# Optimization experiments

Measured on AMD Instinct MI355X. Metric: run time of the kernel, lower is better.

## Reference

```python
import jax, jax.numpy as jnp
import numpy as np

N = 102400       # total nodes (1024 graphs x 100 nodes)
E = 1638400      # edges (avg degree 16)
B = 1024         # graphs; also GRU sequence length (unbatched 2D GRU input)
F_IN, HID, H1 = 4, 16, 6
OUT, FC1, RNN, ACT = 32, 64, 64, 11


def _gat(x, src, dst, W, a_src, a_dst, b, heads, out_dim, concat):
    # PyG GATConv (eval mode, dropout off), add_self_loops=True
    n = x.shape[0]
    loop = jnp.arange(n, dtype=src.dtype)
    s = jnp.concatenate([src, loop])
    d = jnp.concatenate([dst, loop])
    h = (x @ W.T).reshape(n, heads, out_dim)                 # [N,H,F]
    a_s = (h * a_src).sum(-1)                                # [N,H]
    a_d = (h * a_dst).sum(-1)                                # [N,H]
    e = jax.nn.leaky_relu(a_s[s] + a_d[d], 0.2)              # [E',H]
    m = jax.ops.segment_max(e, d, num_segments=n)
    p = jnp.exp(e - m[d])
    alpha = p / jax.ops.segment_sum(p, d, num_segments=n)[d]
    agg = jax.ops.segment_sum(h[s] * alpha[:, :, None], d, num_segments=n)  # [N,H,F]
    agg = agg.reshape(n, heads * out_dim) if concat else agg.mean(axis=1)
    return agg + b


def _gru(xs, wih, whh, bih, bhh):
    # torch nn.GRU, unbatched: xs is [L, FC1], h0 = zeros
    def step(hp, xt):
        gi = xt @ wih.T + bih
        gh = hp @ whh.T + bhh
        ir, iz, i_n = jnp.split(gi, 3)
        hr, hz, h_n = jnp.split(gh, 3)
        r = jax.nn.sigmoid(ir + hr)
        z = jax.nn.sigmoid(iz + hz)
        ng = jnp.tanh(i_n + r * h_n)
        h = (1.0 - z) * ng + z * hp
        return h, h
    _, ys = jax.lax.scan(step, jnp.zeros((RNN,), xs.dtype), xs)
    return ys


def setup_inputs():
    key = jax.random.key(0)
    ks = jax.random.split(key, 16)
    g = lambda i, shape, fan: jax.random.normal(ks[i], shape, jnp.float32) / np.sqrt(fan)
    x = jax.random.normal(ks[0], (N, F_IN), jnp.float32)
    src = jax.random.randint(ks[1], (E,), 0, N)
    dst = jax.random.randint(ks[2], (E,), 0, N)
    dst = jnp.where(dst == src, (dst + 1) % N, dst)  # no pre-existing self-loops
    edge_index = jnp.stack([src, dst]).astype(jnp.int32)
    robot_index = (jnp.arange(B) * (N // B)).astype(jnp.int32)  # ptr[:-1]
    robot_features = jax.random.normal(ks[3], (B, 4), jnp.float32)
    return dict(
        x=x, edge_index=edge_index, robot_index=robot_index, robot_features=robot_features,
        c1_W=g(4, (H1 * HID, F_IN), F_IN), c1_as=g(5, (H1, HID), HID), c1_ad=g(6, (H1, HID), HID),
        c1_b=jnp.zeros((H1 * HID,), jnp.float32),
        c2_W=g(7, (OUT, H1 * HID), H1 * HID), c2_as=g(8, (1, OUT), OUT), c2_ad=g(9, (1, OUT), OUT),
        c2_b=jnp.zeros((OUT,), jnp.float32),
        fc1_W=g(10, (FC1, OUT + 4), OUT + 4), fc1_b=jnp.zeros((FC1,), jnp.float32),
        gru_wih=g(11, (3 * RNN, FC1), FC1), gru_whh=g(12, (3 * RNN, RNN), RNN),
        gru_bih=jnp.zeros((3 * RNN,), jnp.float32), gru_bhh=jnp.zeros((3 * RNN,), jnp.float32),
        fc2_W=g(13, (ACT, RNN), RNN), fc2_b=jnp.zeros((ACT,), jnp.float32),
    )


def reference(x, edge_index, robot_index, robot_features,
              c1_W, c1_as, c1_ad, c1_b, c2_W, c2_as, c2_ad, c2_b,
              fc1_W, fc1_b, gru_wih, gru_whh, gru_bih, gru_bhh, fc2_W, fc2_b):
    src, dst = edge_index[0], edge_index[1]
    h = _gat(x, src, dst, c1_W, c1_as, c1_ad, c1_b, H1, HID, True)   # [N, 96]
    h = jnp.tanh(h)
    h = _gat(h, src, dst, c2_W, c2_as, c2_ad, c2_b, 1, OUT, False)   # [N, 32]
    h = h[robot_index]                                               # [B, 32]
    h = jnp.tanh(jnp.concatenate([h, robot_features], axis=1) @ fc1_W.T + fc1_b)  # [B, 64]
    h = _gru(h, gru_wih, gru_whh, gru_bih, gru_bhh)                  # [B, 64]
    return h @ fc2_W.T + fc2_b                                       # [B, 11] logits
```

## Files before the change

kernel.cpp:

```cpp
#include <hip/hip_runtime.h>

#define S2CAP 24576
#define ECAP  524288

__device__ __forceinline__ float fsig(float x){ return 1.f/(1.f + __expf(-x)); }
__device__ __forceinline__ float ftanh(float a){
  a = fminf(fmaxf(a, -15.f), 15.f);
  float e2 = __expf(2.f*a);
  return (e2 - 1.f)/(e2 + 1.f);
}
__device__ __forceinline__ float attw(float e){
  e = (e > 0.f) ? e : 0.2f*e;
  return __expf(e);
}

__global__ void k_init(const float* __restrict__ c1W, const float* __restrict__ c1as,
                       const float* __restrict__ c1ad, float* __restrict__ AsAd,
                       const int* __restrict__ rix, int B, int* __restrict__ sidx,
                       int* __restrict__ nodeof, int* __restrict__ ctrl,
                       int* __restrict__ cnt1){
  int gid = blockIdx.x*blockDim.x + threadIdx.x;
  if (gid == 0) ctrl[0] = B;
  if (gid < 48){
    int which = gid/24, r = gid%24, k = r/6, h = r%6;
    const float* av = which ? c1ad : c1as;
    float s = 0.f;
    for (int f = 0; f < 16; ++f) s += c1W[(h*16+f)*4 + k] * av[h*16+f];
    AsAd[which*24 + k*6 + h] = s;
  }
  if (gid < B){ int r = rix[gid]; sidx[r] = gid; nodeof[gid] = r; }
  if (gid < S2CAP) cnt1[gid] = 0;
}

__global__ void k_claim(const int* __restrict__ ei, int E, int B,
                        int* __restrict__ sidx, int* __restrict__ nodeof,
                        int* __restrict__ ctrl){
  int e = blockIdx.x*blockDim.x + threadIdx.x;
  if (e >= E) return;
  int d = ei[E + e];
  int sd = sidx[d];
  if (sd < 0 || sd >= B) return;
  int s = ei[e];
  if (sidx[s] < 0){
    int old = atomicCAS(&sidx[s], -1, -2);
    if (old == -1){
      int id = atomicAdd(&ctrl[0], 1);
      if (id < S2CAP){ nodeof[id] = s; sidx[s] = id; }
      else sidx[s] = -1;
    }
  }
}

__global__ void k_count(const int* __restrict__ ei, int E,
                        const int* __restrict__ sidx, int* __restrict__ cnt1){
  int e = blockIdx.x*blockDim.x + threadIdx.x;
  if (e >= E) return;
  int sd = sidx[ei[E + e]];
  if (sd >= 0) atomicAdd(&cnt1[sd], 1);
}

__global__ void k_scan(const int* __restrict__ cnt, int* __restrict__ off,
                       int* __restrict__ run, int n){
  __shared__ int part[1024];
  int tid = threadIdx.x;
  int per = (n + 1023)/1024;
  int base = tid*per;
  int s = 0;
  for (int i = 0; i < per; ++i){ int idx = base+i; if (idx < n) s += cnt[idx]; }
  part[tid] = s; __syncthreads();
  for (int d = 1; d < 1024; d <<= 1){
    int v = part[tid];
    int o = (tid >= d) ? part[tid-d] : 0;
    __syncthreads();
    part[tid] = v + o;
    __syncthreads();
  }
  int acc = (tid == 0) ? 0 : part[tid-1];
  for (int i = 0; i < per; ++i){
    int idx = base+i;
    if (idx < n){ off[idx] = acc; run[idx] = acc; acc += cnt[idx]; }
  }
}

__global__ void k_scatter(const int* __restrict__ ei, int E,
                          const int* __restrict__ sidx, int* __restrict__ run1,
                          int* __restrict__ csr1){
  int e = blockIdx.x*blockDim.x + threadIdx.x;
  if (e >= E) return;
  int sd = sidx[ei[E + e]];
  if (sd >= 0){
    int p = atomicAdd(&run1[sd], 1);
    if (p < ECAP) csr1[p] = ei[e];
  }
}

__global__ void k_gat1(const float* __restrict__ x, const float* __restrict__ c1W,
                       const float* __restrict__ c1b, const float* __restrict__ AsAd,
                       const int* __restrict__ nodeof, const int* __restrict__ off1,
                       const int* __restrict__ cnt1, const int* __restrict__ csr1,
                       const int* __restrict__ ctrl, float* __restrict__ tbuf){
  int gid = blockIdx.x*blockDim.x + threadIdx.x;
  int sid = gid/6, h = gid - sid*6;
  if (sid >= ctrl[0]) return;
  float Ask[4], Adk[4];
  #pragma unroll
  for (int k = 0; k < 4; ++k){ Ask[k] = AsAd[k*6+h]; Adk[k] = AsAd[24 + k*6 + h]; }
  float W[16][4];
  #pragma unroll
  for (int f = 0; f < 16; ++f)
    #pragma unroll
    for (int k = 0; k < 4; ++k) W[f][k] = c1W[(h*16+f)*4 + k];
  int d = nodeof[sid];
  float4 xd = *(const float4*)(x + 4*(size_t)d);
  float ad = xd.x*Adk[0] + xd.y*Adk[1] + xd.z*Adk[2] + xd.w*Adk[3];
  int beg = off1[sid], n = cnt1[sid];
  if (beg >= ECAP) n = 0; else if (beg + n > ECAP) n = ECAP - beg;
  float den = 0.f, agg[16];
  #pragma unroll
  for (int f = 0; f < 16; ++f) agg[f] = 0.f;
  for (int j = -1; j < n; ++j){
    int s = (j < 0) ? d : csr1[beg + j];
    float4 xv = *(const float4*)(x + 4*(size_t)s);
    float as = xv.x*Ask[0] + xv.y*Ask[1] + xv.z*Ask[2] + xv.w*Ask[3];
    float wgt = attw(as + ad);
    den += wgt;
    #pragma unroll
    for (int f = 0; f < 16; ++f){
      float h1 = xv.x*W[f][0] + xv.y*W[f][1] + xv.z*W[f][2] + xv.w*W[f][3];
      agg[f] = fmaf(wgt, h1, agg[f]);
    }
  }
  float inv = 1.f/den;
  #pragma unroll
  for (int f = 0; f < 16; ++f)
    tbuf[(size_t)sid*96 + h*16 + f] = ftanh(agg[f]*inv + c1b[h*16+f]);
}

__global__ void k_h2att(const float* __restrict__ c2W, const float* __restrict__ tbuf,
                        const float* __restrict__ c2as, const float* __restrict__ c2ad,
                        const int* __restrict__ ctrl, float* __restrict__ h2,
                        float* __restrict__ as2, float* __restrict__ ad2){
  int gid = blockIdx.x*blockDim.x + threadIdx.x;
  int sid = gid >> 5, o = gid & 31;
  bool act = sid < ctrl[0];
  float s = 0.f;
  if (act){
    const float* t = tbuf + (size_t)sid*96;
    const float* wr = c2W + o*96;
    #pragma unroll
    for (int j = 0; j < 96; ++j) s = fmaf(wr[j], t[j], s);
    h2[(size_t)sid*32 + o] = s;
  }
  float a = act ? s*c2as[o] : 0.f;
  float b = act ? s*c2ad[o] : 0.f;
  #pragma unroll
  for (int w = 16; w >= 1; w >>= 1){
    a += __shfl_xor(a, w, 32);
    b += __shfl_xor(b, w, 32);
  }
  if (act && o == 0){ as2[sid] = a; ad2[sid] = b; }
}

__global__ void k_gat2fc1(const float* __restrict__ h2, const float* __restrict__ as2,
                          const float* __restrict__ ad2, const float* __restrict__ c2b,
                          const float* __restrict__ rf, const float* __restrict__ fc1W,
                          const float* __restrict__ fc1b, const int* __restrict__ sidx,
                          const int* __restrict__ off1, const int* __restrict__ cnt1,
                          const int* __restrict__ csr1, float* __restrict__ xs, int B){
  int rp = blockIdx.x*blockDim.x + threadIdx.x;
  if (rp >= B) return;
  float ad = ad2[rp];
  float den = 0.f, agg[32];
  #pragma unroll
  for (int o = 0; o < 32; ++o) agg[o] = 0.f;
  int beg = off1[rp], n = cnt1[rp];
  if (beg >= ECAP) n = 0; else if (beg + n > ECAP) n = ECAP - beg;
  for (int j = -1; j < n; ++j){
    int ss;
    if (j < 0) ss = rp;
    else { int s = csr1[beg + j]; ss = sidx[s]; if (ss < 0 || ss >= S2CAP) continue; }
    float wgt = attw(as2[ss] + ad);
    den += wgt;
    const float* hv = h2 + (size_t)ss*32;
    #pragma unroll
    for (int o = 0; o < 32; ++o) agg[o] = fmaf(wgt, hv[o], agg[o]);
  }
  float inv = 1.f/den;
  float cat[36];
  #pragma unroll
  for (int o = 0; o < 32; ++o) cat[o] = agg[o]*inv + c2b[o];
  #pragma unroll
  for (int k = 0; k < 4; ++k) cat[32+k] = rf[rp*4+k];
  for (int o = 0; o < 64; ++o){
    float s = fc1b[o];
    const float* wrow = fc1W + o*36;
    #pragma unroll
    for (int j = 0; j < 36; ++j) s = fmaf(wrow[j], cat[j], s);
    xs[(size_t)rp*64 + o] = ftanh(s);
  }
}

__global__ void k_giT(const float* __restrict__ xs, const float* __restrict__ wih,
                      const float* __restrict__ bih, const float* __restrict__ bhh,
                      float* __restrict__ gi, const float* __restrict__ whh,
                      float* __restrict__ whhT, int B){
  int gid = blockIdx.x*blockDim.x + threadIdx.x;
  int NGI = B*192;
  if (gid < NGI){
    int t = gid/192, g = gid - t*192;
    const float* xv = xs + (size_t)t*64;
    const float* wr = wih + (size_t)g*64;
    float s = bih[g] + (g < 128 ? bhh[g] : 0.f);
    #pragma unroll
    for (int k = 0; k < 64; ++k) s = fmaf(wr[k], xv[k], s);
    gi[gid] = s;
  } else {
    int q = gid - NGI;
    if (q < 192*64){
      int g = q >> 6, k = q & 63;
      whhT[k*192 + g] = whh[g*64 + k];
    }
  }
}

__global__ __launch_bounds__(64) void k_gru(const float* __restrict__ gi,
                       const float* __restrict__ whhT, const float* __restrict__ bhh,
                       float* __restrict__ ys, int B){
  int u = threadIdx.x;
  float wr[64], wz[64], wn[64];
  #pragma unroll
  for (int k = 0; k < 64; ++k){
    wr[k] = whhT[k*192 + u];
    wz[k] = whhT[k*192 + 64 + u];
    wn[k] = whhT[k*192 + 128 + u];
  }
  #pragma unroll
  for (int k = 0; k < 64; ++k){
    asm volatile("" : "+v"(wr[k]), "+v"(wz[k]), "+v"(wn[k]));
  }
  float bn = bhh[128 + u];
  float hu = 0.f;
  float grc = gi[u], gzc = gi[64 + u], gnc = gi[128 + u];
  for (int t = 0; t < B; ++t){
    int tn = (t + 1 < B) ? t + 1 : t;
    float grn = gi[tn*192 + u], gzn = gi[tn*192 + 64 + u], gnn = gi[tn*192 + 128 + u];
    float ar0 = 0.f, ar1 = 0.f, az0 = 0.f, az1 = 0.f, an0 = bn, an1 = 0.f;
    #pragma unroll
    for (int k = 0; k < 64; k += 2){
      float h0 = __int_as_float(__builtin_amdgcn_readlane(__float_as_int(hu), k));
      float h1 = __int_as_float(__builtin_amdgcn_readlane(__float_as_int(hu), k + 1));
      ar0 = fmaf(wr[k],   h0, ar0);
      az0 = fmaf(wz[k],   h0, az0);
      an0 = fmaf(wn[k],   h0, an0);
      ar1 = fmaf(wr[k+1], h1, ar1);
      az1 = fmaf(wz[k+1], h1, az1);
      an1 = fmaf(wn[k+1], h1, an1);
    }
    float r  = fsig(grc + ar0 + ar1);
    float z  = fsig(gzc + az0 + az1);
    float ng = ftanh(gnc + r*(an0 + an1));
    hu = (1.f - z)*ng + z*hu;
    ys[(size_t)t*64 + u] = hu;
    grc = grn; gzc = gzn; gnc = gnn;
  }
}

__global__ void k_fc2(const float* __restrict__ ys, const float* __restrict__ f2W,
                      const float* __restrict__ f2b, float* __restrict__ out, int B){
  int gid = blockIdx.x*blockDim.x + threadIdx.x;
  if (gid >= B*11) return;
  int t = gid/11, a = gid - t*11;
  const float* hv = ys + (size_t)t*64;
  const float* wr = f2W + a*64;
  float s = f2b[a];
  #pragma unroll
  for (int k = 0; k < 64; ++k) s = fmaf(wr[k], hv[k], s);
  out[gid] = s;
}

extern "C" void kernel_launch(void* const* d_in, const int* in_sizes, int n_in,
                              void* d_out, int out_size, void* d_ws, size_t ws_size,
                              hipStream_t stream) {
  (void)n_in; (void)out_size; (void)ws_size;
  const float* x    = (const float*)d_in[0];
  const int*   ei   = (const int*)d_in[1];
  const int*   rix  = (const int*)d_in[2];
  const float* rf   = (const float*)d_in[3];
  const float* c1W  = (const float*)d_in[4];
  const float* c1as = (const float*)d_in[5];
  const float* c1ad = (const float*)d_in[6];
  const float* c1b  = (const float*)d_in[7];
  const float* c2W  = (const float*)d_in[8];
  const float* c2as = (const float*)d_in[9];
  const float* c2ad = (const float*)d_in[10];
  const float* c2b  = (const float*)d_in[11];
  const float* fc1W = (const float*)d_in[12];
  const float* fc1b = (const float*)d_in[13];
  const float* wih  = (const float*)d_in[14];
  const float* whh  = (const float*)d_in[15];
  const float* bih  = (const float*)d_in[16];
  const float* bhh  = (const float*)d_in[17];
  const float* f2W  = (const float*)d_in[18];
  const float* f2b  = (const float*)d_in[19];
  float* out = (float*)d_out;

  const int N = in_sizes[0]/4;
  const int E = in_sizes[1]/2;
  const int B = in_sizes[2];

  char* w = (char*)d_ws;
  size_t off = 0;
  auto take = [&](size_t bytes)->char*{
    char* p = w + off;
    off = (off + bytes + 255) & ~(size_t)255;
    return p;
  };
  int*   ctrl   = (int*)  take(256);
  float* AsAd   = (float*)take(256);
  int*   sidx   = (int*)  take((size_t)N*4);
  int*   nodeof = (int*)  take((size_t)S2CAP*4);
  int*   cnt1   = (int*)  take((size_t)S2CAP*4);
  int*   off1   = (int*)  take((size_t)S2CAP*4);
  int*   run1   = (int*)  take((size_t)S2CAP*4);
  int*   csr1   = (int*)  take((size_t)ECAP*4);
  float* tbuf   = (float*)take((size_t)S2CAP*96*4);
  float* h2     = (float*)take((size_t)S2CAP*32*4);
  float* as2    = (float*)take((size_t)S2CAP*4);
  float* ad2    = (float*)take((size_t)S2CAP*4);
  float* xs     = (float*)take((size_t)B*64*4);
  float* gi     = (float*)take((size_t)B*192*4);
  float* whhT   = (float*)take((size_t)192*64*4);
  float* ys     = (float*)take((size_t)B*64*4);

  hipMemsetAsync(sidx, 0xFF, (size_t)N*4, stream);

  k_init   <<<(S2CAP+255)/256, 256, 0, stream>>>(c1W, c1as, c1ad, AsAd, rix, B, sidx, nodeof, ctrl, cnt1);
  k_claim  <<<(E+255)/256, 256, 0, stream>>>(ei, E, B, sidx, nodeof, ctrl);
  k_count  <<<(E+255)/256, 256, 0, stream>>>(ei, E, sidx, cnt1);
  k_scan   <<<1, 1024, 0, stream>>>(cnt1, off1, run1, S2CAP);
  k_scatter<<<(E+255)/256, 256, 0, stream>>>(ei, E, sidx, run1, csr1);
  k_gat1   <<<(S2CAP*6+255)/256, 256, 0, stream>>>(x, c1W, c1b, AsAd, nodeof, off1, cnt1, csr1, ctrl, tbuf);
  k_h2att  <<<(S2CAP*32+255)/256, 256, 0, stream>>>(c2W, tbuf, c2as, c2ad, ctrl, h2, as2, ad2);
  k_gat2fc1<<<(B+255)/256, 256, 0, stream>>>(h2, as2, ad2, c2b, rf, fc1W, fc1b, sidx, off1, cnt1, csr1, xs, B);
  k_giT    <<<(B*192 + 192*64 + 255)/256, 256, 0, stream>>>(xs, wih, bih, bhh, gi, whh, whhT, B);
  k_gru    <<<1, 64, 0, stream>>>(gi, whhT, bhh, ys, B);
  k_fc2    <<<(B*11+255)/256, 256, 0, stream>>>(ys, f2W, f2b, out, B);
}
```

Measured before the change: 1.082 ms.

## Use fixed-degree edge buckets and split GRU gates across three wavefronts

The count/scan/scatter CSR build is replaced by a single scatter pass into fixed-capacity per-node buckets of 96 slots, removing two kernels including a single-block scan. The GRU recurrence moves from one 64-thread wave computing all three gate dot products to 192 threads, one per gate row, which exchange partial results through double-buffered shared memory with a barrier each step. This shortens the per-step serial FMA chain but adds a block-wide sync per timestep, and any node with more than 96 in-edges silently loses neighbors.

Result: faster. 954.4 us (-11.8%).

```diff
diff --git a/kernel.cpp b/kernel.cpp
--- a/kernel.cpp
+++ b/kernel.cpp
@@ -1,7 +1,7 @@
 #include <hip/hip_runtime.h>
 
 #define S2CAP 24576
-#define ECAP  524288
+#define DEG   96
 
 __device__ __forceinline__ float fsig(float x){ return 1.f/(1.f + __expf(-x)); }
 __device__ __forceinline__ float ftanh(float a){
@@ -51,54 +51,23 @@
   }
 }
 
-__global__ void k_count(const int* __restrict__ ei, int E,
-                        const int* __restrict__ sidx, int* __restrict__ cnt1){
-  int e = blockIdx.x*blockDim.x + threadIdx.x;
-  if (e >= E) return;
-  int sd = sidx[ei[E + e]];
-  if (sd >= 0) atomicAdd(&cnt1[sd], 1);
-}
-
-__global__ void k_scan(const int* __restrict__ cnt, int* __restrict__ off,
-                       int* __restrict__ run, int n){
-  __shared__ int part[1024];
-  int tid = threadIdx.x;
-  int per = (n + 1023)/1024;
-  int base = tid*per;
-  int s = 0;
-  for (int i = 0; i < per; ++i){ int idx = base+i; if (idx < n) s += cnt[idx]; }
-  part[tid] = s; __syncthreads();
-  for (int d = 1; d < 1024; d <<= 1){
-    int v = part[tid];
-    int o = (tid >= d) ? part[tid-d] : 0;
-    __syncthreads();
-    part[tid] = v + o;
-    __syncthreads();
-  }
-  int acc = (tid == 0) ? 0 : part[tid-1];
-  for (int i = 0; i < per; ++i){
-    int idx = base+i;
-    if (idx < n){ off[idx] = acc; run[idx] = acc; acc += cnt[idx]; }
-  }
-}
-
-__global__ void k_scatter(const int* __restrict__ ei, int E,
-                          const int* __restrict__ sidx, int* __restrict__ run1,
-                          int* __restrict__ csr1){
+__global__ void k_scat(const int* __restrict__ ei, int E,
+                       const int* __restrict__ sidx, int* __restrict__ cnt1,
+                       int* __restrict__ csr1){
   int e = blockIdx.x*blockDim.x + threadIdx.x;
   if (e >= E) return;
   int sd = sidx[ei[E + e]];
   if (sd >= 0){
-    int p = atomicAdd(&run1[sd], 1);
-    if (p < ECAP) csr1[p] = ei[e];
+    int p = atomicAdd(&cnt1[sd], 1);
+    if (p < DEG) csr1[sd*DEG + p] = ei[e];
   }
 }
 
 __global__ void k_gat1(const float* __restrict__ x, const float* __restrict__ c1W,
                        const float* __restrict__ c1b, const float* __restrict__ AsAd,
-                       const int* __restrict__ nodeof, const int* __restrict__ off1,
-                       const int* __restrict__ cnt1, const int* __restrict__ csr1,
-                       const int* __restrict__ ctrl, float* __restrict__ tbuf){
+                       const int* __restrict__ nodeof, const int* __restrict__ cnt1,
+                       const int* __restrict__ csr1, const int* __restrict__ ctrl,
+                       float* __restrict__ tbuf){
   int gid = blockIdx.x*blockDim.x + threadIdx.x;
   int sid = gid/6, h = gid - sid*6;
   if (sid >= ctrl[0]) return;
@@ -113,8 +82,8 @@
   int d = nodeof[sid];
   float4 xd = *(const float4*)(x + 4*(size_t)d);
   float ad = xd.x*Adk[0] + xd.y*Adk[1] + xd.z*Adk[2] + xd.w*Adk[3];
-  int beg = off1[sid], n = cnt1[sid];
-  if (beg >= ECAP) n = 0; else if (beg + n > ECAP) n = ECAP - beg;
+  int beg = sid*DEG, n = cnt1[sid];
+  n = (n < DEG) ? n : DEG;
   float den = 0.f, agg[16];
   #pragma unroll
   for (int f = 0; f < 16; ++f) agg[f] = 0.f;
@@ -165,16 +134,16 @@
                           const float* __restrict__ ad2, const float* __restrict__ c2b,
                           const float* __restrict__ rf, const float* __restrict__ fc1W,
                           const float* __restrict__ fc1b, const int* __restrict__ sidx,
-                          const int* __restrict__ off1, const int* __restrict__ cnt1,
-                          const int* __restrict__ csr1, float* __restrict__ xs, int B){
+                          const int* __restrict__ cnt1, const int* __restrict__ csr1,
+                          float* __restrict__ xs, int B){
   int rp = blockIdx.x*blockDim.x + threadIdx.x;
   if (rp >= B) return;
   float ad = ad2[rp];
   float den = 0.f, agg[32];
   #pragma unroll
   for (int o = 0; o < 32; ++o) agg[o] = 0.f;
-  int beg = off1[rp], n = cnt1[rp];
-  if (beg >= ECAP) n = 0; else if (beg + n > ECAP) n = ECAP - beg;
+  int beg = rp*DEG, n = cnt1[rp];
+  n = (n < DEG) ? n : DEG;
   for (int j = -1; j < n; ++j){
     int ss;
     if (j < 0) ss = rp;
@@ -223,45 +192,51 @@
   }
 }
 
-__global__ __launch_bounds__(64) void k_gru(const float* __restrict__ gi,
+__global__ __launch_bounds__(192, 1) void k_gru3(const float* __restrict__ gi,
                        const float* __restrict__ whhT, const float* __restrict__ bhh,
                        float* __restrict__ ys, int B){
-  int u = threadIdx.x;
-  float wr[64], wz[64], wn[64];
-  #pragma unroll
-  for (int k = 0; k < 64; ++k){
-    wr[k] = whhT[k*192 + u];
-    wz[k] = whhT[k*192 + 64 + u];
-    wn[k] = whhT[k*192 + 128 + u];
-  }
-  #pragma unroll
-  for (int k = 0; k < 64; ++k){
-    asm volatile("" : "+v"(wr[k]), "+v"(wz[k]), "+v"(wn[k]));
-  }
-  float bn = bhh[128 + u];
-  float hu = 0.f;
-  float grc = gi[u], gzc = gi[64 + u], gnc = gi[128 + u];
+  int tid = threadIdx.x;
+  int w = tid >> 6, u = tid & 63, g = tid;
+  float wv[64];
+  #pragma unroll
+  for (int k = 0; k < 64; ++k) wv[k] = whhT[k*192 + g];
+  float bb = (w == 2) ? bhh[128 + u] : 0.f;
+  __shared__ float rzbuf[2][256];
+  float hvec = 0.f;
+  float gcur = gi[g];
   for (int t = 0; t < B; ++t){
     int tn = (t + 1 < B) ? t + 1 : t;
-    float grn = gi[tn*192 + u], gzn = gi[tn*192 + 64 + u], gnn = gi[tn*192 + 128 + u];
-    float ar0 = 0.f, ar1 = 0.f, az0 = 0.f, az1 = 0.f, an0 = bn, an1 = 0.f;
-    #pragma unroll
-    for (int k = 0; k < 64; k += 2){
-      float h0 = __int_as_float(__builtin_amdgcn_readlane(__float_as_int(hu), k));
-      float h1 = __int_as_float(__builtin_amdgcn_readlane(__float_as_int(hu), k + 1));
-      ar0 = fmaf(wr[k],   h0, ar0);
-      az0 = fmaf(wz[k],   h0, az0);
-      an0 = fmaf(wn[k],   h0, an0);
-      ar1 = fmaf(wr[k+1], h1, ar1);
-      az1 = fmaf(wz[k+1], h1, az1);
-      an1 = fmaf(wn[k+1], h1, an1);
-    }
-    float r  = fsig(grc + ar0 + ar1);
-    float z  = fsig(gzc + az0 + az1);
-    float ng = ftanh(gnc + r*(an0 + an1));
-    hu = (1.f - z)*ng + z*hu;
-    ys[(size_t)t*64 + u] = hu;
-    grc = grn; gzc = gzn; gnc = gnn;
+    float gnext = gi[tn*192 + g];
+    float a0 = 0.f, a1 = 0.f, a2 = 0.f, a3 = 0.f;
+    int hb = __float_as_int(hvec);
+    #pragma unroll
+    for (int k = 0; k < 64; k += 4){
+      float h0 = __int_as_float(__builtin_amdgcn_readlane(hb, k));
+      float h1 = __int_as_float(__builtin_amdgcn_readlane(hb, k + 1));
+      float h2 = __int_as_float(__builtin_amdgcn_readlane(hb, k + 2));
+      float h3 = __int_as_float(__builtin_amdgcn_readlane(hb, k + 3));
+      a0 = fmaf(wv[k],     h0, a0);
+      a1 = fmaf(wv[k + 1], h1, a1);
+      a2 = fmaf(wv[k + 2], h2, a2);
+      a3 = fmaf(wv[k + 3], h3, a3);
+    }
+    float dot = (a0 + a1) + (a2 + a3);
+    float* buf = rzbuf[t & 1];
+    if (w < 2){
+      buf[w*64 + u] = gcur + dot;
+    } else {
+      buf[128 + u] = dot + bb;
+      buf[192 + u] = gcur;
+    }
+    __syncthreads();
+    float pre_r = buf[u], pre_z = buf[64 + u], an = buf[128 + u], i_n = buf[192 + u];
+    float r  = fsig(pre_r);
+    float z  = fsig(pre_z);
+    float ng = ftanh(i_n + r*an);
+    float hnew = (1.f - z)*ng + z*hvec;
+    if (w == 2) ys[(size_t)t*64 + u] = hnew;
+    hvec = hnew;
+    gcur = gnext;
   }
 }
 
@@ -320,9 +295,7 @@
   int*   sidx   = (int*)  take((size_t)N*4);
   int*   nodeof = (int*)  take((size_t)S2CAP*4);
   int*   cnt1   = (int*)  take((size_t)S2CAP*4);
-  int*   off1   = (int*)  take((size_t)S2CAP*4);
-  int*   run1   = (int*)  take((size_t)S2CAP*4);
-  int*   csr1   = (int*)  take((size_t)ECAP*4);
+  int*   csr1   = (int*)  take((size_t)S2CAP*DEG*4);
   float* tbuf   = (float*)take((size_t)S2CAP*96*4);
   float* h2     = (float*)take((size_t)S2CAP*32*4);
   float* as2    = (float*)take((size_t)S2CAP*4);
@@ -336,13 +309,11 @@
 
   k_init   <<<(S2CAP+255)/256, 256, 0, stream>>>(c1W, c1as, c1ad, AsAd, rix, B, sidx, nodeof, ctrl, cnt1);
   k_claim  <<<(E+255)/256, 256, 0, stream>>>(ei, E, B, sidx, nodeof, ctrl);
-  k_count  <<<(E+255)/256, 256, 0, stream>>>(ei, E, sidx, cnt1);
-  k_scan   <<<1, 1024, 0, stream>>>(cnt1, off1, run1, S2CAP);
-  k_scatter<<<(E+255)/256, 256, 0, stream>>>(ei, E, sidx, run1, csr1);
-  k_gat1   <<<(S2CAP*6+255)/256, 256, 0, stream>>>(x, c1W, c1b, AsAd, nodeof, off1, cnt1, csr1, ctrl, tbuf);
+  k_scat   <<<(E+255)/256, 256, 0, stream>>>(ei, E, sidx, cnt1, csr1);
+  k_gat1   <<<(S2CAP*6+255)/256, 256, 0, stream>>>(x, c1W, c1b, AsAd, nodeof, cnt1, csr1, ctrl, tbuf);
   k_h2att  <<<(S2CAP*32+255)/256, 256, 0, stream>>>(c2W, tbuf, c2as, c2ad, ctrl, h2, as2, ad2);
-  k_gat2fc1<<<(B+255)/256, 256, 0, stream>>>(h2, as2, ad2, c2b, rf, fc1W, fc1b, sidx, off1, cnt1, csr1, xs, B);
+  k_gat2fc1<<<(B+255)/256, 256, 0, stream>>>(h2, as2, ad2, c2b, rf, fc1W, fc1b, sidx, cnt1, csr1, xs, B);
   k_giT    <<<(B*192 + 192*64 + 255)/256, 256, 0, stream>>>(xs, wih, bih, bhh, gi, whh, whhT, B);
-  k_gru    <<<1, 64, 0, stream>>>(gi, whhT, bhh, ys, B);
+  k_gru3   <<<1, 192, 0, stream>>>(gi, whhT, bhh, ys, B);
   k_fc2    <<<(B*11+255)/256, 256, 0, stream>>>(ys, f2W, f2b, out, B);
 }
```
